# Kernel optimization log

Hardware: AMD Instinct MI355X
Metric: run time of the kernel (lower is better)

## Reference

```python
import jax, jax.numpy as jnp
import numpy as np

CH = 16
HID = 128
UPDATE_RATE = 0.25

def _perception_kernel():
    identity = jnp.array([[0.,0.,0.],[0.,1.,0.],[0.,0.,0.]], jnp.float32)
    sobel_x = jnp.array([[-1.,0.,1.],[-2.,0.,2.],[-1.,0.,1.]], jnp.float32)
    sobel_y = sobel_x.T
    laplacian = jnp.array([[1.,1.,1.],[1.,-8.,1.],[1.,1.,1.]], jnp.float32)
    k = jnp.stack([identity, sobel_x, sobel_y, laplacian])[:, None, :, :]  # [4,1,3,3]
    return jnp.tile(k, (CH, 1, 1, 1))  # [4*CH,1,3,3], OIHW depthwise

def setup_inputs() -> dict:
    key = jax.random.key(0)
    ks = jax.random.split(key, 10)
    B, H, W = 32, 256, 256
    x = jax.random.normal(ks[0], (B, CH, H, W), jnp.float32)
    # 1x1 conv weights: stored as [out,in]; biases [out]
    def lin(k, o, i, scale):
        return jax.random.normal(k, (o, i), jnp.float32) * scale
    w1 = lin(ks[1], HID, CH*4, 1.0/np.sqrt(CH*4)); b1 = jnp.zeros((HID,), jnp.float32)
    w2 = lin(ks[2], HID, HID, 1.0/np.sqrt(HID)); b2 = jnp.zeros((HID,), jnp.float32)
    w3 = lin(ks[3], HID, HID, 1.0/np.sqrt(HID)); b3 = jnp.zeros((HID,), jnp.float32)
    # last layer initialized to zero in original; use small random so gradients flow meaningfully
    w4 = lin(ks[4], CH, HID, 0.01)
    # precomputed random update mask (torch.rand < rate), constant w.r.t. grads
    update_mask = (jax.random.uniform(ks[5], (B, 1, H, W)) < UPDATE_RATE).astype(jnp.float32)
    return {"x": x, "w1": w1, "b1": b1, "w2": w2, "b2": b2, "w3": w3, "b3": b3, "w4": w4, "update_mask": update_mask, "steps": 1}

def _alive_mask(x, threshold=0.01):
    alpha = x[:, :2, :, :]
    pool = jax.lax.reduce_window(alpha, -jnp.inf, jax.lax.max,
                                 (1, 1, 3, 3), (1, 1, 1, 1),
                                 ((0, 0), (0, 0), (1, 1), (1, 1)))
    s = jnp.sum(jnp.abs(pool), axis=1, keepdims=True)  # [B,1,H,W]
    return (s > threshold).astype(x.dtype)

def _step(x, params, update_mask, kernel):
    w1, b1, w2, b2, w3, b3, w4 = params
    pre_alive = _alive_mask(x)
    # depthwise 3x3 perception conv: [B,CH,H,W] -> [B,4*CH,H,W]
    y = jax.lax.conv_general_dilated(x, kernel, (1, 1), ((1, 1), (1, 1)),
                                     dimension_numbers=('NCHW', 'OIHW', 'NCHW'),
                                     feature_group_count=CH)
    lrelu = lambda z: jax.nn.leaky_relu(z, 0.01)
    h = lrelu(jnp.einsum('oc,bchw->bohw', w1, y) + b1[None, :, None, None])
    h = lrelu(jnp.einsum('oc,bchw->bohw', w2, h) + b2[None, :, None, None])
    h = lrelu(jnp.einsum('oc,bchw->bohw', w3, h) + b3[None, :, None, None])
    dy = jnp.einsum('oc,bchw->bohw', w4, h)
    x = x + dy * update_mask
    post_alive = _alive_mask(x)
    return x * (pre_alive * post_alive)

def reference(x, w1, b1, w2, b2, w3, b3, w4, update_mask, steps):
    kernel = _perception_kernel()
    params = (w1, b1, w2, b2, w3, b3, w4)
    for _ in range(steps):
        x = _step(x, params, update_mask, kernel)
    return x
```

## Files before the change

### kernel.cpp

```cpp
#include <hip/hip_runtime.h>

typedef _Float16 f16;
typedef f16 f16x2 __attribute__((ext_vector_type(2)));
typedef f16 f16x8 __attribute__((ext_vector_type(8)));
typedef __fp16 h2v __attribute__((ext_vector_type(2)));
typedef float f32x4 __attribute__((ext_vector_type(4)));
typedef float f32x16 __attribute__((ext_vector_type(16)));
typedef unsigned int uint;
typedef unsigned short ushort;
typedef unsigned long long ull;

#define NCH 16
#define NB 32
#define NH 256
#define NW 256
#define HW 65536
#define CHW 1048576

#define BIAS_BYTE 90112
#define WS_BYTES 91648
#define BAND_ROWS 5
#define STAGE_ROWS 7
#define XBAND_OFF WS_BYTES
#define XBAND_BYTES (STAGE_ROWS*256*32)
#define LIST_OFF (XBAND_OFF + XBAND_BYTES)
#define LIST_MAX (BAND_ROWS*256)
#define CTR_OFF (LIST_OFF + LIST_MAX*2)
#define LDS_TOTAL (CTR_OFF + 16)
#define NBANDS_PER_IMG 52
#define NBANDS_TOTAL (NB*NBANDS_PER_IMG)

__global__ void prep_k(const float* __restrict__ w1, const float* __restrict__ w2,
                       const float* __restrict__ w3, const float* __restrict__ w4,
                       const float* __restrict__ b1, const float* __restrict__ b2,
                       const float* __restrict__ b3, float* __restrict__ wsf) {
  f16* wf = (f16*)wsf;
  int id = blockIdx.x * 256 + threadIdx.x;
  if (id < 8192) {
    int j = id & 7, l = (id >> 3) & 63, mt = (id >> 9) & 3, kt = id >> 11;
    int o = mt * 32 + (l & 31), c = kt * 16 + (l >> 5) * 8 + j;
    wf[id] = (f16)w1[o * 64 + c];
  } else if (id < 24576) {
    int t = id - 8192;
    int j = t & 7, l = (t >> 3) & 63, mt = (t >> 9) & 3, kt = t >> 11;
    int o = mt * 32 + (l & 31), c = kt * 16 + (l >> 5) * 8 + j;
    wf[8192 + t] = (f16)w2[o * 128 + c];
  } else if (id < 40960) {
    int t = id - 24576;
    int j = t & 7, l = (t >> 3) & 63, mt = (t >> 9) & 3, kt = t >> 11;
    int o = mt * 32 + (l & 31), c = kt * 16 + (l >> 5) * 8 + j;
    wf[24576 + t] = (f16)w3[o * 128 + c];
  } else if (id < 45056) {
    int t = id - 40960;
    int j = t & 7, l = (t >> 3) & 63, kt = t >> 9;
    int m = l & 31, hh = l >> 5;
    int c = kt * 16 + hh * 8 + j;
    wf[40960 + t] = (m < 16) ? (f16)w4[m * 128 + c] : (f16)0.f;
  } else if (id < 45440) {
    int t = id - 45056;
    int r = t & 15, hh = (t >> 4) & 1, mt = (t >> 5) & 3, ly = t >> 7;
    const float* bb = (ly == 0) ? b1 : (ly == 1) ? b2 : b3;
    ((float*)((unsigned char*)wsf + BIAS_BYTE))[t] =
        bb[mt * 32 + (r & 3) + 8 * (r >> 2) + 4 * hh];
  }
}

__global__ __launch_bounds__(256)
void copy_k(const float4* __restrict__ x4, float4* __restrict__ xn4) {
  const size_t total = (size_t)NB * CHW / 4;
  for (size_t i = (size_t)blockIdx.x * 256 + threadIdx.x; i < total; i += (size_t)2048 * 256)
    xn4[i] = x4[i];
}

__device__ __forceinline__ void pl32swap(uint& a, uint& b) {
  asm volatile("v_permlane32_swap_b32 %0, %1" : "+v"(a), "+v"(b));
}

__device__ __forceinline__ f16x8 mk8(uint a, uint b, uint c, uint d) {
  union { uint u[4]; f16x8 v; } z;
  z.u[0] = a; z.u[1] = b; z.u[2] = c; z.u[3] = d;
  return z.v;
}

template <int NKT>
__device__ __forceinline__ void gemm_half(const unsigned char* __restrict__ smem,
                                          int wfFragBase, int biasFloatOff, int lane, int hi,
                                          const f16x8* __restrict__ B, f32x16 acc[4]) {
#pragma unroll
  for (int mt = 0; mt < 4; ++mt) {
    const f32x16* bp =
        (const f32x16*)(smem + BIAS_BYTE + 4 * (biasFloatOff + (mt * 2 + hi) * 16));
    acc[mt] = *bp;
  }
  const f16x8* A = (const f16x8*)smem + wfFragBase + lane;
  __builtin_amdgcn_s_setprio(1);
#pragma unroll
  for (int kt = 0; kt < NKT; ++kt) {
#pragma unroll
    for (int mt = 0; mt < 4; ++mt) {
      f16x8 a = A[(kt * 4 + mt) * 64];
      acc[mt] = __builtin_amdgcn_mfma_f32_32x32x16_f16(a, B[kt], acc[mt], 0, 0, 0);
    }
  }
  __builtin_amdgcn_s_setprio(0);
}

__device__ __forceinline__ void epilogue_swap(const f32x16 acc[4], f16x8 Bn[8]) {
  uint w[32];
  const h2v c001 = {(__fp16)0.01f, (__fp16)0.01f};
#pragma unroll
  for (int mt = 0; mt < 4; ++mt) {
#pragma unroll
    for (int i = 0; i < 8; ++i) {
      h2v u = __builtin_amdgcn_cvt_pkrtz(acc[mt][2 * i], acc[mt][2 * i + 1]);
      h2v s = u * c001;
      h2v m = __builtin_elementwise_max(u, s);
      w[mt * 8 + i] = __builtin_bit_cast(uint, m);
    }
  }
#pragma unroll
  for (int kt = 0; kt < 8; ++kt) {
    int mt = kt >> 1, sub = kt & 1;
    int W = mt * 8 + sub * 4;
    uint a0 = w[W], a1 = w[W + 1], a2 = w[W + 2], a3 = w[W + 3];
    pl32swap(a0, a2);
    pl32swap(a1, a3);
    Bn[kt] = mk8(a0, a1, a2, a3);
  }
}

__device__ __forceinline__ void perc_band(const unsigned char* __restrict__ xband,
                                          int rl, int c, int hi, f16x8 B1h[4]) {
  const bool fL = c > 0, fR = c < NW - 1;
  const int cm = fL ? c - 1 : c, cp2 = fR ? c + 1 : c;
  const int swm = (hi ^ (cm & 1)) << 4;
  const int swc = (hi ^ (c & 1)) << 4;
  const int swp = (hi ^ (cp2 & 1)) << 4;
  union U4 { uint4 u; f16 hh[8]; };
  U4 q[9];
#pragma unroll
  for (int dr = 0; dr < 3; ++dr) {
    const unsigned char* rowp = xband + (size_t)(rl + dr) * 256 * 32;
    q[dr * 3 + 0].u = *(const uint4*)(rowp + cm * 32 + swm);
    q[dr * 3 + 1].u = *(const uint4*)(rowp + c * 32 + swc);
    q[dr * 3 + 2].u = *(const uint4*)(rowp + cp2 * 32 + swp);
  }
  uint yw[16];
#pragma unroll
  for (int j = 0; j < 8; ++j) {
    float v00 = (float)q[0].hh[j], v01 = (float)q[1].hh[j], v02 = (float)q[2].hh[j];
    float v10 = (float)q[3].hh[j], v11 = (float)q[4].hh[j], v12 = (float)q[5].hh[j];
    float v20 = (float)q[6].hh[j], v21 = (float)q[7].hh[j], v22 = (float)q[8].hh[j];
    if (!fL) { v00 = 0.f; v10 = 0.f; v20 = 0.f; }
    if (!fR) { v02 = 0.f; v12 = 0.f; v22 = 0.f; }
    float rs0 = v00 + v01 + v02, rs2 = v20 + v21 + v22;
    float fsx = (v02 - v00) + (v22 - v20) + 2.f * (v12 - v10);
    float fsy = (rs2 - rs0) + (v21 - v01);
    float flap = (rs0 + rs2 + v10 + v12) - 8.f * v11;
    h2v t0 = __builtin_amdgcn_cvt_pkrtz(v11, fsx);
    h2v t1 = __builtin_amdgcn_cvt_pkrtz(fsy, flap);
    int kt = j >> 1, cp = j & 1;
    yw[kt * 4 + cp * 2 + 0] = __builtin_bit_cast(uint, t0);
    yw[kt * 4 + cp * 2 + 1] = __builtin_bit_cast(uint, t1);
  }
#pragma unroll
  for (int kt = 0; kt < 4; ++kt)
    B1h[kt] = mk8(yw[kt * 4], yw[kt * 4 + 1], yw[kt * 4 + 2], yw[kt * 4 + 3]);
}

__global__ __launch_bounds__(768, 1)
void nca_band_k(const float* __restrict__ x, const float* __restrict__ wsf,
                const float* __restrict__ mask, float* __restrict__ xn) {
  extern __shared__ unsigned char smem[];
  unsigned char* xband = smem + XBAND_OFF;
  ushort* list = (ushort*)(smem + LIST_OFF);
  int* ctr = (int*)(smem + CTR_OFF);

  const int tid = threadIdx.x;
  const int lane = tid & 63;
  const int wv = tid >> 6;
  const int hi = lane >> 5;

  {
    const uint4* src = (const uint4*)wsf;
    uint4* dst = (uint4*)smem;
    for (int i = tid; i < WS_BYTES / 16; i += 768) dst[i] = src[i];
  }
  __syncthreads();

  for (int band = blockIdx.x; band < NBANDS_TOTAL; band += 256) {
    const int b = band / NBANDS_PER_IMG;
    const int r0 = (band - b * NBANDS_PER_IMG) * BAND_ROWS;
    const float* xb = x + (size_t)b * CHW;
    float* xnb = xn + (size_t)b * CHW;
    const float* mb = mask + (size_t)b * HW;

    if (tid == 0) *ctr = 0;
    __syncthreads();

    for (int e = tid; e < STAGE_ROWS * 2 * 256; e += 768) {
      int col = e & 255;
      int pair = e >> 8;
      int sr = pair >> 1;
      int h = pair & 1;
      int gr = r0 - 1 + sr;
      union { f16 hh[8]; uint4 u; } rec;
      if ((unsigned)gr < (unsigned)NH) {
#pragma unroll
        for (int j = 0; j < 8; ++j) {
          int ch = ((j >> 1) << 2) | (h << 1) | (j & 1);
          rec.hh[j] = (f16)xb[((size_t)ch << 16) + (gr << 8) + col];
        }
      } else {
        rec.u.x = 0; rec.u.y = 0; rec.u.z = 0; rec.u.w = 0;
      }
      *(uint4*)(xband + (size_t)(sr * 256 + col) * 32 + ((h ^ (col & 1)) << 4)) = rec.u;
    }

    if (wv < BAND_ROWS) {
      int row = r0 + wv;
      if (row < NH) {
        ull bal[4];
        int c = 0;
#pragma unroll
        for (int k = 0; k < 4; ++k) {
          bool a = mb[(row << 8) + k * 64 + lane] > 0.f;
          bal[k] = __ballot(a);
          c += __popcll(bal[k]);
        }
        int base;
        if (lane == 0) base = atomicAdd(ctr, c);
        base = __shfl(base, 0);
#pragma unroll
        for (int k = 0; k < 4; ++k) {
          int rank = __popcll(bal[k] & ((1ull << lane) - 1));
          if ((bal[k] >> lane) & 1ull)
            list[base + rank] = (ushort)((wv << 8) | (k * 64 + lane));
          base += __popcll(bal[k]);
        }
      }
    }
    __syncthreads();

    const int n = *ctr;
    const int nbatch = (n + 31) >> 5;
    for (int k = wv; k < nbatch; k += 12) {
      int idx = k * 32 + (lane & 31);
      if (idx >= n) idx = n - 1;
      const int entry = list[idx];
      const int rl = entry >> 8, c = entry & 255;

      f16x8 B1[4];
      perc_band(xband, rl, c, hi, B1);

      f32x16 acc[4];
      f16x8 B2[8], B3[8], B4[8];
      gemm_half<4>(smem, 0, 0, lane, hi, B1, acc);
      epilogue_swap(acc, B2);
      gemm_half<8>(smem, 1024, 128, lane, hi, B2, acc);
      epilogue_swap(acc, B3);
      gemm_half<8>(smem, 3072, 256, lane, hi, B3, acc);
      epilogue_swap(acc, B4);

      f32x16 a4;
#pragma unroll
      for (int r = 0; r < 16; ++r) a4[r] = 0.f;
      {
        const f16x8* A4 = (const f16x8*)smem + 5120 + lane;
        __builtin_amdgcn_s_setprio(1);
#pragma unroll
        for (int kt = 0; kt < 8; ++kt)
          a4 = __builtin_amdgcn_mfma_f32_32x32x16_f16(A4[kt * 64], B4[kt], a4, 0, 0, 0);
        __builtin_amdgcn_s_setprio(0);
      }

      {
        const int row = r0 + rl;
        const float* xrb = xb + (row << 8) + c;
        float* xob = xnb + (row << 8) + c;
#pragma unroll
        for (int r = 0; r < 8; ++r) {
          int ch = (r & 3) + 8 * (r >> 2) + 4 * hi;
          xob[(size_t)ch << 16] = xrb[(size_t)ch << 16] + a4[r];
        }
      }
    }
    __syncthreads();
  }
}

__global__ void alive_scale_k(const float* __restrict__ x, float* __restrict__ xn) {
  __shared__ float pm[4][258];
  const int col = threadIdx.x;
  const int row = blockIdx.x;
  const int b = blockIdx.y;
  const float NEG = -3.0e38f;
  float v0 = NEG, v1 = NEG, v2 = NEG, v3 = NEG;
  const size_t base0 = (size_t)b * CHW + ((size_t)row << 8) + col;
#pragma unroll
  for (int dr = -1; dr <= 1; ++dr) {
    int rr = row + dr;
    if ((unsigned)rr < NH) {
      long o = (long)base0 + dr * NW;
      v0 = fmaxf(v0, x[o]);
      v1 = fmaxf(v1, x[o + HW]);
      v2 = fmaxf(v2, xn[o]);
      v3 = fmaxf(v3, xn[o + HW]);
    }
  }
  pm[0][col + 1] = v0;
  pm[1][col + 1] = v1;
  pm[2][col + 1] = v2;
  pm[3][col + 1] = v3;
  if (col == 0) {
#pragma unroll
    for (int f = 0; f < 4; ++f) { pm[f][0] = NEG; pm[f][257] = NEG; }
  }
  __syncthreads();
  float p0 = fmaxf(fmaxf(pm[0][col], pm[0][col + 1]), pm[0][col + 2]);
  float p1 = fmaxf(fmaxf(pm[1][col], pm[1][col + 1]), pm[1][col + 2]);
  float p2 = fmaxf(fmaxf(pm[2][col], pm[2][col + 1]), pm[2][col + 2]);
  float p3 = fmaxf(fmaxf(pm[3][col], pm[3][col + 1]), pm[3][col + 2]);
  bool alive = ((fabsf(p0) + fabsf(p1)) > 0.01f) && ((fabsf(p2) + fabsf(p3)) > 0.01f);
  if (!alive) {
#pragma unroll
    for (int ch = 0; ch < NCH; ++ch) xn[base0 + ((size_t)ch << 16)] = 0.f;
  }
}

extern "C" void kernel_launch(void* const* d_in, const int* in_sizes, int n_in,
                              void* d_out, int out_size, void* d_ws, size_t ws_size,
                              hipStream_t stream) {
  const float* x    = (const float*)d_in[0];
  const float* w1   = (const float*)d_in[1];
  const float* b1   = (const float*)d_in[2];
  const float* w2   = (const float*)d_in[3];
  const float* b2   = (const float*)d_in[4];
  const float* w3   = (const float*)d_in[5];
  const float* b3   = (const float*)d_in[6];
  const float* w4   = (const float*)d_in[7];
  const float* mask = (const float*)d_in[8];

  float* wsf = (float*)d_ws;
  float* xn = (float*)d_out;

  hipFuncSetAttribute(reinterpret_cast<const void*>(nca_band_k),
                      hipFuncAttributeMaxDynamicSharedMemorySize, LDS_TOTAL);

  prep_k<<<178, 256, 0, stream>>>(w1, w2, w3, w4, b1, b2, b3, wsf);
  copy_k<<<2048, 256, 0, stream>>>((const float4*)x, (float4*)xn);
  nca_band_k<<<256, 768, LDS_TOTAL, stream>>>(x, wsf, mask, xn);
  alive_scale_k<<<dim3(NH, NB), 256, 0, stream>>>(x, xn);
}
```

Measured before the change: 183.3 us.

## Prefetch next band into registers, fuse passthrough copy, widen block to 1024

Drops the separate full-tensor copy kernel. The band kernel now writes unchanged values itself, only for pixels whose update mask is off. The next band's x records and mask values are loaded into registers before the current band's MLP work and written to LDS afterwards, with double-buffered compaction lists and flags, so global-load latency is hidden behind compute. The block size goes from 768 to 1024 threads (16 waves), which raises register pressure and adds live prefetch registers during the GEMM chain.

```diff
diff --git a/kernel.cpp b/kernel.cpp
--- a/kernel.cpp
+++ b/kernel.cpp
@@ -1,7 +1,6 @@
 #include <hip/hip_runtime.h>
 
 typedef _Float16 f16;
-typedef f16 f16x2 __attribute__((ext_vector_type(2)));
 typedef f16 f16x8 __attribute__((ext_vector_type(8)));
 typedef __fp16 h2v __attribute__((ext_vector_type(2)));
 typedef float f32x4 __attribute__((ext_vector_type(4)));
@@ -23,12 +22,14 @@
 #define STAGE_ROWS 7
 #define XBAND_OFF WS_BYTES
 #define XBAND_BYTES (STAGE_ROWS*256*32)
+#define LIST_MAX 1280
 #define LIST_OFF (XBAND_OFF + XBAND_BYTES)
-#define LIST_MAX (BAND_ROWS*256)
-#define CTR_OFF (LIST_OFF + LIST_MAX*2)
-#define LDS_TOTAL (CTR_OFF + 16)
+#define FLAG_OFF (LIST_OFF + 2*LIST_MAX*2)
+#define NACT_OFF (FLAG_OFF + 2*1280)
+#define LDS_TOTAL (NACT_OFF + 16)
 #define NBANDS_PER_IMG 52
 #define NBANDS_TOTAL (NB*NBANDS_PER_IMG)
+#define NRECS (STAGE_ROWS*2*256)
 
 __global__ void prep_k(const float* __restrict__ w1, const float* __restrict__ w2,
                        const float* __restrict__ w3, const float* __restrict__ w4,
@@ -65,13 +66,6 @@
   }
 }
 
-__global__ __launch_bounds__(256)
-void copy_k(const float4* __restrict__ x4, float4* __restrict__ xn4) {
-  const size_t total = (size_t)NB * CHW / 4;
-  for (size_t i = (size_t)blockIdx.x * 256 + threadIdx.x; i < total; i += (size_t)2048 * 256)
-    xn4[i] = x4[i];
-}
-
 __device__ __forceinline__ void pl32swap(uint& a, uint& b) {
   asm volatile("v_permlane32_swap_b32 %0, %1" : "+v"(a), "+v"(b));
 }
@@ -168,13 +162,67 @@
     B1h[kt] = mk8(yw[kt * 4], yw[kt * 4 + 1], yw[kt * 4 + 2], yw[kt * 4 + 3]);
 }
 
-__global__ __launch_bounds__(768, 1)
+__device__ __forceinline__ uint4 load_rec(const float* __restrict__ xb, int r0,
+                                          int e) {
+  int col = e & 255;
+  int pair = e >> 8;
+  int sr = pair >> 1, h = pair & 1;
+  int gr = r0 - 1 + sr;
+  union { f16 hh[8]; uint4 u; } rc;
+  if ((unsigned)gr < (unsigned)NH) {
+#pragma unroll
+    for (int j = 0; j < 8; ++j) {
+      int ch = ((j >> 1) << 2) | (h << 1) | (j & 1);
+      rc.hh[j] = (f16)xb[((size_t)ch << 16) + (gr << 8) + col];
+    }
+  } else {
+    rc.u.x = 0; rc.u.y = 0; rc.u.z = 0; rc.u.w = 0;
+  }
+  return rc.u;
+}
+
+__device__ __forceinline__ void write_rec(unsigned char* __restrict__ xband, int e,
+                                          uint4 r) {
+  int col = e & 255;
+  int pair = e >> 8;
+  int sr = pair >> 1, h = pair & 1;
+  *(uint4*)(xband + (size_t)(sr * 256 + col) * 32 + ((h ^ (col & 1)) << 4)) = r;
+}
+
+__device__ __forceinline__ void compact_row(const float mv[4], int wv, int lane, int row,
+                                            ushort* __restrict__ list,
+                                            unsigned char* __restrict__ flags,
+                                            int* __restrict__ ctr) {
+  if (row >= NH) return;
+  ull bal[4];
+  int c = 0;
+#pragma unroll
+  for (int k = 0; k < 4; ++k) {
+    bool a = mv[k] > 0.f;
+    flags[wv * 256 + k * 64 + lane] = a ? 1 : 0;
+    bal[k] = __ballot(a);
+    c += __popcll(bal[k]);
+  }
+  int base;
+  if (lane == 0) base = atomicAdd(ctr, c);
+  base = __shfl(base, 0);
+#pragma unroll
+  for (int k = 0; k < 4; ++k) {
+    int rank = __popcll(bal[k] & ((1ull << lane) - 1));
+    if ((bal[k] >> lane) & 1ull)
+      list[base + rank] = (ushort)((wv << 8) | (k * 64 + lane));
+    base += __popcll(bal[k]);
+  }
+}
+
+__global__ __launch_bounds__(1024, 1)
 void nca_band_k(const float* __restrict__ x, const float* __restrict__ wsf,
                 const float* __restrict__ mask, float* __restrict__ xn) {
   extern __shared__ unsigned char smem[];
   unsigned char* xband = smem + XBAND_OFF;
-  ushort* list = (ushort*)(smem + LIST_OFF);
-  int* ctr = (int*)(smem + CTR_OFF);
+  ushort* listbuf = (ushort*)(smem + LIST_OFF);
+  unsigned char* flagbuf = smem + FLAG_OFF;
+  int* nacts = (int*)(smem + NACT_OFF);
 
   const int tid = threadIdx.x;
   const int lane = tid & 63;
@@ -184,67 +232,80 @@
   {
     const uint4* src = (const uint4*)wsf;
     uint4* dst = (uint4*)smem;
-    for (int i = tid; i < WS_BYTES / 16; i += 768) dst[i] = src[i];
-  }
+    for (int i = tid; i < WS_BYTES / 16; i += 1024) dst[i] = src[i];
+  }
+  if (tid < 2) nacts[tid] = 0;
   __syncthreads();
 
-  for (int band = blockIdx.x; band < NBANDS_TOTAL; band += 256) {
-    const int b = band / NBANDS_PER_IMG;
-    const int r0 = (band - b * NBANDS_PER_IMG) * BAND_ROWS;
+  {
+    const int band = blockIdx.x;
+    const int b = band / NBANDS_PER_IMG, r0 = (band % NBANDS_PER_IMG) * BAND_ROWS;
+    const float* xb = x + (size_t)b * CHW;
+#pragma unroll
+    for (int i = 0; i < 4; ++i) {
+      int e = tid + i * 1024;
+      if (e < NRECS) write_rec(xband, e, load_rec(xb, r0, e));
+    }
+    if (wv < BAND_ROWS) {
+      int row = r0 + wv;
+      float mv[4] = {0.f, 0.f, 0.f, 0.f};
+      if (row < NH) {
+        const float* mb = mask + (size_t)b * HW;
+#pragma unroll
+        for (int k = 0; k < 4; ++k) mv[k] = mb[(row << 8) + k * 64 + lane];
+      }
+      compact_row(mv, wv, lane, row, listbuf, flagbuf, &nacts[0]);
+    }
+  }
+  __syncthreads();
+
+  for (int band = blockIdx.x, t = 0; band < NBANDS_TOTAL; band += 256, ++t) {
+    const int lb = t & 1;
+    const int b = band / NBANDS_PER_IMG, r0 = (band % NBANDS_PER_IMG) * BAND_ROWS;
     const float* xb = x + (size_t)b * CHW;
     float* xnb = xn + (size_t)b * CHW;
-    const float* mb = mask + (size_t)b * HW;
-
-    if (tid == 0) *ctr = 0;
-    __syncthreads();
-
-    for (int e = tid; e < STAGE_ROWS * 2 * 256; e += 768) {
+    const ushort* list = listbuf + lb * LIST_MAX;
+    const unsigned char* flags = flagbuf + lb * 1280;
+    const int n = nacts[lb];
+
+    const int nxt = band + 256;
+    const bool hasNext = nxt < NBANDS_TOTAL;
+    uint4 rec[4];
+    float nmv[4] = {0.f, 0.f, 0.f, 0.f};
+    if (hasNext) {
+      const int b2 = nxt / NBANDS_PER_IMG, nr0 = (nxt % NBANDS_PER_IMG) * BAND_ROWS;
+      const float* nxb = x + (size_t)b2 * CHW;
+#pragma unroll
+      for (int i = 0; i < 4; ++i) {
+        int e = tid + i * 1024;
+        if (e < NRECS) rec[i] = load_rec(nxb, nr0, e);
+      }
+      if (wv < BAND_ROWS) {
+        int row = nr0 + wv;
+        if (row < NH) {
+          const float* nmb = mask + (size_t)b2 * HW;
+#pragma unroll
+          for (int k = 0; k < 4; ++k) nmv[k] = nmb[(row << 8) + k * 64 + lane];
+        }
+      }
+    }
+    __builtin_amdgcn_sched_barrier(0);
+
+#pragma unroll
+    for (int i = 0; i < 20; ++i) {
+      int e = tid + i * 1024;
       int col = e & 255;
-      int pair = e >> 8;
-      int sr = pair >> 1;
-      int h = pair & 1;
-      int gr = r0 - 1 + sr;
-      union { f16 hh[8]; uint4 u; } rec;
-      if ((unsigned)gr < (unsigned)NH) {
-#pragma unroll
-        for (int j = 0; j < 8; ++j) {
-          int ch = ((j >> 1) << 2) | (h << 1) | (j & 1);
-          rec.hh[j] = (f16)xb[((size_t)ch << 16) + (gr << 8) + col];
-        }
-      } else {
-        rec.u.x = 0; rec.u.y = 0; rec.u.z = 0; rec.u.w = 0;
-      }
-      *(uint4*)(xband + (size_t)(sr * 256 + col) * 32 + ((h ^ (col & 1)) << 4)) = rec.u;
-    }
-
-    if (wv < BAND_ROWS) {
-      int row = r0 + wv;
-      if (row < NH) {
-        ull bal[4];
-        int c = 0;
-#pragma unroll
-        for (int k = 0; k < 4; ++k) {
-          bool a = mb[(row << 8) + k * 64 + lane] > 0.f;
-          bal[k] = __ballot(a);
-          c += __popcll(bal[k]);
-        }
-        int base;
-        if (lane == 0) base = atomicAdd(ctr, c);
-        base = __shfl(base, 0);
-#pragma unroll
-        for (int k = 0; k < 4; ++k) {
-          int rank = __popcll(bal[k] & ((1ull << lane) - 1));
-          if ((bal[k] >> lane) & 1ull)
-            list[base + rank] = (ushort)((wv << 8) | (k * 64 + lane));
-          base += __popcll(bal[k]);
-        }
-      }
-    }
-    __syncthreads();
-
-    const int n = *ctr;
+      int t2 = e >> 8;
+      int rl = t2 >> 4, ch = t2 & 15;
+      int row = r0 + rl;
+      if (row < NH && !flags[rl * 256 + col]) {
+        size_t off = ((size_t)ch << 16) + (row << 8) + col;
+        xnb[off] = xb[off];
+      }
+    }
+
     const int nbatch = (n + 31) >> 5;
-    for (int k = wv; k < nbatch; k += 12) {
+    for (int k = wv; k < nbatch; k += 16) {
       int idx = k * 32 + (lane & 31);
       if (idx >= n) idx = n - 1;
       const int entry = list[idx];
@@ -285,7 +346,24 @@
         }
       }
     }
+
+    if (tid == 0) nacts[lb ^ 1] = 0;
     __syncthreads();
+
+    if (hasNext) {
+      const int nr0 = ((band + 256) % NBANDS_PER_IMG) * BAND_ROWS;
+#pragma unroll
+      for (int i = 0; i < 4; ++i) {
+        int e = tid + i * 1024;
+        if (e < NRECS) write_rec(xband, e, rec[i]);
+      }
+      if (wv < BAND_ROWS) {
+        int row = nr0 + wv;
+        compact_row(nmv, wv, lane, row, listbuf + (lb ^ 1) * LIST_MAX,
+                    flagbuf + (lb ^ 1) * 1280, &nacts[lb ^ 1]);
+      }
+      __syncthreads();
+    }
   }
 }
 
@@ -348,7 +426,6 @@
                       hipFuncAttributeMaxDynamicSharedMemorySize, LDS_TOTAL);
 
   prep_k<<<178, 256, 0, stream>>>(w1, w2, w3, w4, b1, b2, b3, wsf);
-  copy_k<<<2048, 256, 0, stream>>>((const float4*)x, (float4*)xn);
-  nca_band_k<<<256, 768, LDS_TOTAL, stream>>>(x, wsf, mask, xn);
+  nca_band_k<<<256, 1024, LDS_TOTAL, stream>>>(x, wsf, mask, xn);
   alive_scale_k<<<dim3(NH, NB), 256, 0, stream>>>(x, xn);
 }
```

After: 293.0 us. +59.9%, slower.

## Drop full input copy; fill masked-off pixels in final alive-scaling pass

Applied to the files above, without the earlier changes.

Removes the kernel that copied all of x into the output before the band kernel ran. The final pass now reads the update mask: for pixels with no update it takes x as the post-update state, writing x where the cell is alive and zero where it is not. This saves a full read and write of the tensor, roughly 128MB each way. The cost is an extra mask read and four per-pixel branches, and it relies on the band kernel writing only the masked pixels.

```diff
diff --git a/kernel.cpp b/kernel.cpp
--- a/kernel.cpp
+++ b/kernel.cpp
@@ -1,7 +1,6 @@
 #include <hip/hip_runtime.h>
 
 typedef _Float16 f16;
-typedef f16 f16x2 __attribute__((ext_vector_type(2)));
 typedef f16 f16x8 __attribute__((ext_vector_type(8)));
 typedef __fp16 h2v __attribute__((ext_vector_type(2)));
 typedef float f32x4 __attribute__((ext_vector_type(4)));
@@ -65,13 +64,6 @@
   }
 }
 
-__global__ __launch_bounds__(256)
-void copy_k(const float4* __restrict__ x4, float4* __restrict__ xn4) {
-  const size_t total = (size_t)NB * CHW / 4;
-  for (size_t i = (size_t)blockIdx.x * 256 + threadIdx.x; i < total; i += (size_t)2048 * 256)
-    xn4[i] = x4[i];
-}
-
 __device__ __forceinline__ void pl32swap(uint& a, uint& b) {
   asm volatile("v_permlane32_swap_b32 %0, %1" : "+v"(a), "+v"(b));
 }
@@ -289,42 +281,82 @@
   }
 }
 
-__global__ void alive_scale_k(const float* __restrict__ x, float* __restrict__ xn) {
-  __shared__ float pm[4][258];
+__global__ __launch_bounds__(256)
+void finish_k(const float* __restrict__ x, const float* __restrict__ mask,
+              float* __restrict__ xn) {
+  __shared__ float xp0[3][258], xp1[3][258], sp0[3][258], sp1[3][258];
   const int col = threadIdx.x;
   const int row = blockIdx.x;
   const int b = blockIdx.y;
   const float NEG = -3.0e38f;
-  float v0 = NEG, v1 = NEG, v2 = NEG, v3 = NEG;
-  const size_t base0 = (size_t)b * CHW + ((size_t)row << 8) + col;
-#pragma unroll
-  for (int dr = -1; dr <= 1; ++dr) {
-    int rr = row + dr;
-    if ((unsigned)rr < NH) {
-      long o = (long)base0 + dr * NW;
-      v0 = fmaxf(v0, x[o]);
-      v1 = fmaxf(v1, x[o + HW]);
-      v2 = fmaxf(v2, xn[o]);
-      v3 = fmaxf(v3, xn[o + HW]);
-    }
-  }
-  pm[0][col + 1] = v0;
-  pm[1][col + 1] = v1;
-  pm[2][col + 1] = v2;
-  pm[3][col + 1] = v3;
+  const float* xb = x + (size_t)b * CHW;
+  float* xnb = xn + (size_t)b * CHW;
+  const float* mb = mask + (size_t)b * HW;
+
+  float mctr = 0.f;
+#pragma unroll
+  for (int dr = 0; dr < 3; ++dr) {
+    int rr = row - 1 + dr;
+    float x0 = NEG, x1 = NEG, s0 = NEG, s1 = NEG;
+    if ((unsigned)rr < (unsigned)NH) {
+      int off = (rr << 8) + col;
+      float m = mb[off];
+      x0 = xb[off];
+      x1 = xb[HW + off];
+      if (m > 0.f) {
+        s0 = xnb[off];
+        s1 = xnb[HW + off];
+      } else {
+        s0 = x0;
+        s1 = x1;
+      }
+      if (dr == 1) mctr = m;
+    }
+    xp0[dr][col + 1] = x0;
+    xp1[dr][col + 1] = x1;
+    sp0[dr][col + 1] = s0;
+    sp1[dr][col + 1] = s1;
+  }
   if (col == 0) {
 #pragma unroll
-    for (int f = 0; f < 4; ++f) { pm[f][0] = NEG; pm[f][257] = NEG; }
+    for (int dr = 0; dr < 3; ++dr) {
+      xp0[dr][0] = NEG; xp0[dr][257] = NEG;
+      xp1[dr][0] = NEG; xp1[dr][257] = NEG;
+      sp0[dr][0] = NEG; sp0[dr][257] = NEG;
+      sp1[dr][0] = NEG; sp1[dr][257] = NEG;
+    }
   }
   __syncthreads();
-  float p0 = fmaxf(fmaxf(pm[0][col], pm[0][col + 1]), pm[0][col + 2]);
-  float p1 = fmaxf(fmaxf(pm[1][col], pm[1][col + 1]), pm[1][col + 2]);
-  float p2 = fmaxf(fmaxf(pm[2][col], pm[2][col + 1]), pm[2][col + 2]);
-  float p3 = fmaxf(fmaxf(pm[3][col], pm[3][col + 1]), pm[3][col + 2]);
-  bool alive = ((fabsf(p0) + fabsf(p1)) > 0.01f) && ((fabsf(p2) + fabsf(p3)) > 0.01f);
-  if (!alive) {
-#pragma unroll
-    for (int ch = 0; ch < NCH; ++ch) xn[base0 + ((size_t)ch << 16)] = 0.f;
+
+  float px0 = NEG, px1 = NEG, ps0 = NEG, ps1 = NEG;
+#pragma unroll
+  for (int dr = 0; dr < 3; ++dr) {
+#pragma unroll
+    for (int dc = 0; dc < 3; ++dc) {
+      px0 = fmaxf(px0, xp0[dr][col + dc]);
+      px1 = fmaxf(px1, xp1[dr][col + dc]);
+      ps0 = fmaxf(ps0, sp0[dr][col + dc]);
+      ps1 = fmaxf(ps1, sp1[dr][col + dc]);
+    }
+  }
+  const bool pre = (fabsf(px0) + fabsf(px1)) > 0.01f;
+  const bool post = (fabsf(ps0) + fabsf(ps1)) > 0.01f;
+  const bool alive = pre && post;
+  const bool active = mctr > 0.f;
+
+  const size_t base = ((size_t)row << 8) + col;
+  if (!active) {
+    if (alive) {
+#pragma unroll
+      for (int ch = 0; ch < NCH; ++ch)
+        xnb[base + ((size_t)ch << 16)] = xb[base + ((size_t)ch << 16)];
+    } else {
+#pragma unroll
+      for (int ch = 0; ch < NCH; ++ch) xnb[base + ((size_t)ch << 16)] = 0.f;
+    }
+  } else if (!alive) {
+#pragma unroll
+    for (int ch = 0; ch < NCH; ++ch) xnb[base + ((size_t)ch << 16)] = 0.f;
   }
 }
 
@@ -348,7 +380,6 @@
                       hipFuncAttributeMaxDynamicSharedMemorySize, LDS_TOTAL);
 
   prep_k<<<178, 256, 0, stream>>>(w1, w2, w3, w4, b1, b2, b3, wsf);
-  copy_k<<<2048, 256, 0, stream>>>((const float4*)x, (float4*)xn);
   nca_band_k<<<256, 768, LDS_TOTAL, stream>>>(x, wsf, mask, xn);
-  alive_scale_k<<<dim3(NH, NB), 256, 0, stream>>>(x, xn);
-}
+  finish_k<<<dim3(NH, NB), 256, 0, stream>>>(x, mask, xn);
+}
```

New measurement: 186.4 us. Within noise of the previous version (+1.7%).
